# Optimization experiments

Hardware: AMD Instinct MI355X
Metric: run time of the kernel (lower is better)

## Reference

```python
import jax, jax.numpy as jnp
import numpy as np


def setup_inputs() -> dict:
    key = jax.random.key(0)
    k1, k2, k3 = jax.random.split(key, 3)
    B, OUT, IN = 256, 512, 512
    x = jax.random.normal(k1, (B, IN), dtype=jnp.float32)
    weight = jax.random.normal(k2, (OUT, IN), dtype=jnp.float32)
    logits = jax.random.normal(k3, (OUT, IN), dtype=jnp.float32)
    return {"x": x, "weight": weight, "logits": logits}


def reference(x, weight, logits):
    # x: [B, IN]; weight/logits: [OUT, IN]
    B = x.shape[0]
    OUT, IN = logits.shape
    kg1, kg2 = jax.random.split(jax.random.key(42))

    # weight property: 2*tanh(_weight) * gumbel_softmax(_logits, hard=True), tau=1
    g1 = jax.random.gumbel(kg1, (OUT, IN), dtype=logits.dtype)
    soft1 = jax.nn.softmax(logits + g1, axis=-1)
    hard1 = jax.nn.one_hot(jnp.argmax(soft1, axis=-1), IN, dtype=soft1.dtype)
    # straight-through: forward value is the one-hot
    mask_hard = hard1 + soft1 - jax.lax.stop_gradient(soft1)
    W_eff = 2.0 * jnp.tanh(2.0 * jnp.tanh(weight) * mask_hard)  # [OUT, IN]

    # per-example soft gumbel-softmax mask over the in-dim, tau=1
    g2 = jax.random.gumbel(kg2, (B, OUT, IN), dtype=logits.dtype)
    L = jax.nn.softmax(logits[None, :, :] + g2, axis=-1)  # [B, OUT, IN]

    # y[b,o] = sum_i W_eff[o,i] * L[b,o,i] * x[b,i]
    y = jnp.einsum('oi,boi,bi->bo', W_eff, L, x)
    return y
```

## Files before the change

kernel.cpp:

```cpp
#include <hip/hip_runtime.h>
#include <stdint.h>


__device__ __forceinline__ float fast_log2(float x) {
  float r; asm("v_log_f32 %0, %1" : "=v"(r) : "v"(x)); return r;
}
__device__ __forceinline__ float fast_exp2(float x) {
  float r; asm("v_exp_f32 %0, %1" : "=v"(r) : "v"(x)); return r;
}
__device__ __forceinline__ float fast_exp(float x) {
  return fast_exp2(x * 1.4426950408889634f);
}
__device__ __forceinline__ float fast_tanh(float w) {
  float t = fast_exp2(w * 2.8853900817779268f);
  return (t - 1.0f) / (t + 1.0f);
}

__device__ __forceinline__ uint32_t rotl32(uint32_t x, int r) {
  return (x << r) | (x >> (32 - r));
}

__device__ __forceinline__ void threefry2x32(uint32_t k0, uint32_t k1,
                                             uint32_t x0, uint32_t x1,
                                             uint32_t& o0, uint32_t& o1) {
  const uint32_t ks2 = k0 ^ k1 ^ 0x1BD11BDAu;
  x0 += k0; x1 += k1;
  const int rotA[4] = {13, 15, 26, 6};
  const int rotB[4] = {17, 29, 16, 24};
#pragma unroll
  for (int g = 0; g < 5; ++g) {
    const int* rots = (g & 1) ? rotB : rotA;
#pragma unroll
    for (int r = 0; r < 4; ++r) {
      x0 += x1; x1 = rotl32(x1, rots[r]); x1 ^= x0;
    }
    const uint32_t ks[3] = {k0, k1, ks2};
    x0 += ks[(g + 1) % 3];
    x1 += ks[(g + 2) % 3] + (uint32_t)(g + 1);
  }
  o0 = x0; o1 = x1;
}

__device__ __forceinline__ uint32_t tf_bits(uint32_t ka, uint32_t kb, uint32_t e) {
  uint32_t r0, r1;
  threefry2x32(ka, kb, 0u, e, r0, r1);
  return r0 ^ r1;
}

__device__ __forceinline__ float gumbel_from_bits(uint32_t bits) {
  float f = __uint_as_float((bits >> 9) | 0x3f800000u) - 1.0f;
  float u = f + 1.17549435e-38f;
  float nl = -0.6931471805599453f * fast_log2(u);
  return -0.6931471805599453f * fast_log2(nl);
}

__global__ __launch_bounds__(256) void k_fused(const float* __restrict__ x,
                                               const float* __restrict__ weight,
                                               const float* __restrict__ logits,
                                               float* __restrict__ out) {
  const int o    = blockIdx.x & 511;
  const int bg   = blockIdx.x >> 9;
  const int tid  = threadIdx.x;
  const int lane = tid & 63;
  const int wid  = tid >> 6;
  const float* lrow = logits + o * 512;

  uint32_t k1a, k1b, k2a, k2b;
  threefry2x32(0u, 42u, 0u, 0u, k1a, k1b);
  threefry2x32(0u, 42u, 0u, 1u, k2a, k2b);

  float v; int idx;
  {
    const uint32_t e0 = (uint32_t)(o * 512 + tid);
    v   = lrow[tid] + gumbel_from_bits(tf_bits(k1a, k1b, e0));
    idx = tid;
    float v2 = lrow[tid + 256] + gumbel_from_bits(tf_bits(k1a, k1b, e0 + 256u));
    if (v2 > v) { v = v2; idx = tid + 256; }
  }
  for (int off = 32; off > 0; off >>= 1) {
    float ov = __shfl_down(v, off);
    int   oi = __shfl_down(idx, off);
    if (ov > v || (ov == v && oi < idx)) { v = ov; idx = oi; }
  }
  __shared__ float swv[4];
  __shared__ int   swi[4];
  __shared__ int   s_istar;
  __shared__ float s_c;
  if (lane == 0) { swv[wid] = v; swi[wid] = idx; }
  __syncthreads();
  if (tid == 0) {
    float bv = swv[0]; int bi = swi[0];
    for (int w = 1; w < 4; ++w)
      if (swv[w] > bv || (swv[w] == bv && swi[w] < bi)) { bv = swv[w]; bi = swi[w]; }
    s_istar = bi;
    s_c = 2.0f * fast_tanh(2.0f * fast_tanh(weight[o * 512 + bi]));
  }
  __syncthreads();
  const int   isel = s_istar;
  const float c    = s_c;

  const int b   = bg * 4 + wid;
  const int row = (b << 9) | o;
  const uint32_t base = (uint32_t)row << 9;

  float sum = 0.0f, selv = 0.0f;
#pragma unroll
  for (int j = 0; j < 8; ++j) {
    const int i = lane + 64 * j;
    float z  = lrow[i] + gumbel_from_bits(tf_bits(k2a, k2b, base + (uint32_t)i));
    float ev = fast_exp(z);
    sum += ev;
    if (i == isel) selv = ev;
  }
  for (int off = 32; off > 0; off >>= 1) {
    sum  += __shfl_down(sum, off);
    selv += __shfl_down(selv, off);
  }
  if (lane == 0) out[row] = c * x[(b << 9) | isel] * selv / sum;
}

extern "C" void kernel_launch(void* const* d_in, const int* in_sizes, int n_in,
                              void* d_out, int out_size, void* d_ws, size_t ws_size,
                              hipStream_t stream) {
  const float* x      = (const float*)d_in[0];
  const float* weight = (const float*)d_in[1];
  const float* logits = (const float*)d_in[2];
  float* out = (float*)d_out;
  k_fused<<<dim3(512 * 64), dim3(256), 0, stream>>>(x, weight, logits, out);
}
```

Measured before the change: 179.1 us.

## Amortize per-row argmax over 64 batch rows per block and fold gumbel constants

The grid shrinks from 32768 to 2048 blocks, and each wave now loops over 16 batch rows. The hard gumbel argmax for an output row and the logits loads are therefore computed once per 64 batches instead of once per 4, which removes most of the redundant threefry and log work in the prologue. The gumbel and exp math is also reworked in base 2 so constants fold into one fma and one exp2. The selected value is fetched with a single shuffle instead of a reduction. The trade-off is fewer blocks and a serial per-wave loop, so less parallelism for latency hiding, plus a small clamp that changes edge-case rounding.

```diff
diff --git a/kernel.cpp b/kernel.cpp
--- a/kernel.cpp
+++ b/kernel.cpp
@@ -8,16 +8,13 @@
 __device__ __forceinline__ float fast_exp2(float x) {
   float r; asm("v_exp_f32 %0, %1" : "=v"(r) : "v"(x)); return r;
 }
-__device__ __forceinline__ float fast_exp(float x) {
-  return fast_exp2(x * 1.4426950408889634f);
-}
 __device__ __forceinline__ float fast_tanh(float w) {
   float t = fast_exp2(w * 2.8853900817779268f);
   return (t - 1.0f) / (t + 1.0f);
 }
 
-__device__ __forceinline__ uint32_t rotl32(uint32_t x, int r) {
-  return (x << r) | (x >> (32 - r));
+__device__ __forceinline__ uint32_t rotl(uint32_t x, int r) {
+  return __builtin_rotateleft32(x, (unsigned)r);
 }
 
 __device__ __forceinline__ void threefry2x32(uint32_t k0, uint32_t k1,
@@ -32,7 +29,7 @@
     const int* rots = (g & 1) ? rotB : rotA;
 #pragma unroll
     for (int r = 0; r < 4; ++r) {
-      x0 += x1; x1 = rotl32(x1, rots[r]); x1 ^= x0;
+      x0 += x1; x1 = rotl(x1, rots[r]); x1 ^= x0;
     }
     const uint32_t ks[3] = {k0, k1, ks2};
     x0 += ks[(g + 1) % 3];
@@ -47,11 +44,12 @@
   return r0 ^ r1;
 }
 
-__device__ __forceinline__ float gumbel_from_bits(uint32_t bits) {
-  float f = __uint_as_float((bits >> 9) | 0x3f800000u) - 1.0f;
-  float u = f + 1.17549435e-38f;
-  float nl = -0.6931471805599453f * fast_log2(u);
-  return -0.6931471805599453f * fast_log2(nl);
+__device__ __forceinline__ float neglog2_from_bits(uint32_t bits) {
+  float f  = __uint_as_float((bits >> 9) | 0x3f800000u) - 1.0f;
+  float u  = f + 1.17549435e-38f;
+  float l1 = fast_log2(u);
+  float nl = fmaxf(-l1, 1e-37f);
+  return fast_log2(nl);
 }
 
 __global__ __launch_bounds__(256) void k_fused(const float* __restrict__ x,
@@ -72,9 +70,13 @@
   float v; int idx;
   {
     const uint32_t e0 = (uint32_t)(o * 512 + tid);
-    v   = lrow[tid] + gumbel_from_bits(tf_bits(k1a, k1b, e0));
+    float g1a = fmaf(-0.69314718056f, neglog2_from_bits(tf_bits(k1a, k1b, e0)),
+                     0.3665129206f);
+    v   = lrow[tid] + g1a;
     idx = tid;
-    float v2 = lrow[tid + 256] + gumbel_from_bits(tf_bits(k1a, k1b, e0 + 256u));
+    float g1b = fmaf(-0.69314718056f, neglog2_from_bits(tf_bits(k1a, k1b, e0 + 256u)),
+                     0.3665129206f);
+    float v2 = lrow[tid + 256] + g1b;
     if (v2 > v) { v = v2; idx = tid + 256; }
   }
   for (int off = 32; off > 0; off >>= 1) {
@@ -99,24 +101,31 @@
   const int   isel = s_istar;
   const float c    = s_c;
 
-  const int b   = bg * 4 + wid;
-  const int row = (b << 9) | o;
-  const uint32_t base = (uint32_t)row << 9;
+  float lsc[8];
+#pragma unroll
+  for (int j = 0; j < 8; ++j)
+    lsc[j] = fmaf(lrow[lane + 64 * j], 1.4426950408889634f, 0.5287663729f);
 
-  float sum = 0.0f, selv = 0.0f;
+  const int b0 = bg * 64 + wid * 16;
+#pragma unroll 1
+  for (int it = 0; it < 16; ++it) {
+    const int b   = b0 + it;
+    const int row = (b << 9) | o;
+    const uint32_t base = (uint32_t)row << 9;
+
+    float sum = 0.0f, selv = 0.0f;
 #pragma unroll
-  for (int j = 0; j < 8; ++j) {
-    const int i = lane + 64 * j;
-    float z  = lrow[i] + gumbel_from_bits(tf_bits(k2a, k2b, base + (uint32_t)i));
-    float ev = fast_exp(z);
-    sum += ev;
-    if (i == isel) selv = ev;
+    for (int j = 0; j < 8; ++j) {
+      const int i = lane + 64 * j;
+      float l2 = neglog2_from_bits(tf_bits(k2a, k2b, base + (uint32_t)i));
+      float ev = fast_exp2(lsc[j] - l2);
+      sum += ev;
+      selv = (i == isel) ? ev : selv;
+    }
+    for (int off = 32; off > 0; off >>= 1) sum += __shfl_down(sum, off);
+    selv = __shfl(selv, isel & 63);
+    if (lane == 0) out[row] = c * x[(b << 9) | isel] * selv / sum;
   }
-  for (int off = 32; off > 0; off >>= 1) {
-    sum  += __shfl_down(sum, off);
-    selv += __shfl_down(selv, off);
-  }
-  if (lane == 0) out[row] = c * x[(b << 9) | isel] * selv / sum;
 }
 
 extern "C" void kernel_launch(void* const* d_in, const int* in_sizes, int n_in,
@@ -126,5 +135,5 @@
   const float* weight = (const float*)d_in[1];
   const float* logits = (const float*)d_in[2];
   float* out = (float*)d_out;
-  k_fused<<<dim3(512 * 64), dim3(256), 0, stream>>>(x, weight, logits, out);
+  k_fused<<<dim3(512 * 4), dim3(256), 0, stream>>>(x, weight, logits, out);
 }
```

Result: no change. 181.5 us (+1.3%).
